# Optimization experiments

Measured on AMD Instinct MI355X. Metric: run time of the kernel, lower is better.

Reference implementation:

```python
import jax, jax.numpy as jnp
import numpy as np

N = 100000   # nodes
E = 1000000  # edges per block
P = 100000   # pos/neg link edges
IN = 128
H = 64


def setup_inputs() -> dict:
    key = jax.random.key(0)
    ks = jax.random.split(key, 24)
    d = {}
    d["x"] = jax.random.normal(ks[0], (N, IN), jnp.float32)
    d["edge_weight"] = jax.random.uniform(ks[1], (3, E), jnp.float32)
    d["src"] = jax.random.randint(ks[2], (E,), 0, N)
    d["dst"] = jax.random.randint(ks[3], (E,), 0, N)
    d["pos_src"] = jax.random.randint(ks[4], (P,), 0, N)
    d["pos_dst"] = jax.random.randint(ks[5], (P,), 0, N)
    d["neg_src"] = jax.random.randint(ks[6], (P,), 0, N)
    d["neg_dst"] = jax.random.randint(ks[7], (P,), 0, N)
    s = 1.0 / np.sqrt(IN)
    h = 1.0 / np.sqrt(H)
    d["W0"] = jax.random.normal(ks[8], (IN, H), jnp.float32) * s
    d["b0"] = jnp.zeros((H,), jnp.float32)
    d["W1"] = jax.random.normal(ks[9], (H, H), jnp.float32) * h
    d["b1"] = jnp.zeros((H,), jnp.float32)
    d["W2"] = jax.random.normal(ks[10], (H, H), jnp.float32) * h
    d["b2"] = jnp.zeros((H,), jnp.float32)
    d["P0"] = jax.random.normal(ks[11], (H, H), jnp.float32) * h
    d["pb0"] = jnp.zeros((H,), jnp.float32)
    d["P1"] = jax.random.normal(ks[12], (H, H), jnp.float32) * h
    d["pb1"] = jnp.zeros((H,), jnp.float32)
    d["P2"] = jax.random.normal(ks[13], (H, 1), jnp.float32) * h
    d["pb2"] = jnp.zeros((1,), jnp.float32)
    return d


def _graph_conv(h, W, b, src, dst, ew, n_nodes):
    # DGL GraphConv, norm='both': D_out^{-1/2} on source feats,
    # edge-weighted sum aggregation, D_in^{-1/2} on result, then linear.
    ones = jnp.ones(src.shape[0], h.dtype)
    deg_out = jax.ops.segment_sum(ones, src, num_segments=n_nodes)
    deg_in = jax.ops.segment_sum(ones, dst, num_segments=n_nodes)
    norm_src = jax.lax.rsqrt(jnp.maximum(deg_out, 1.0))
    norm_dst = jax.lax.rsqrt(jnp.maximum(deg_in, 1.0))
    # apply weight before aggregation (in_feats >= out_feats); math-equivalent either way
    hw = (h * norm_src[:, None]) @ W            # [N, H]
    msg = hw[src] * ew[:, None]                 # [E, H] gather + scale
    agg = jax.ops.segment_sum(msg, dst, num_segments=n_nodes)  # scatter-add
    return agg * norm_dst[:, None] + b


def reference(x, edge_weight, src, dst, pos_src, pos_dst, neg_src, neg_dst,
              W0, b0, W1, b1, W2, b2, P0, pb0, P1, pb1, P2, pb2):
    h = jax.nn.relu(_graph_conv(x, W0, b0, src, dst, edge_weight[0], N))
    h = jax.nn.relu(_graph_conv(h, W1, b1, src, dst, edge_weight[1], N))
    h = _graph_conv(h, W2, b2, src, dst, edge_weight[2], N)  # no relu on last layer

    def mlp(z):
        z = jax.nn.relu(z @ P0 + pb0)
        z = jax.nn.relu(z @ P1 + pb1)
        return z @ P2 + pb2

    h_pos = mlp(h[pos_src] * h[pos_dst])  # [P, 1]
    h_neg = mlp(h[neg_src] * h[neg_dst])  # [P, 1]
    return (h_pos, h_neg)
```

## Files before the change

kernel.cpp:

```cpp
#include <hip/hip_runtime.h>


#define NN 100000
#define NE 1000000
#define NP 100000
#define SCAN_NB 98

__device__ __forceinline__ void row_fma(float4& acc, float xv, const float4& wv) {
    acc.x = fmaf(xv, wv.x, acc.x);
    acc.y = fmaf(xv, wv.y, acc.y);
    acc.z = fmaf(xv, wv.z, acc.z);
    acc.w = fmaf(xv, wv.w, acc.w);
}

__global__ void deg_kernel(const int4* __restrict__ src4, const int4* __restrict__ dst4,
                           int* __restrict__ deg_out, int* __restrict__ deg_in, int E4) {
    int tid = blockIdx.x * blockDim.x + threadIdx.x;
    if (tid < E4) {
        int4 s = src4[tid], d = dst4[tid];
        atomicAdd(&deg_out[s.x], 1);
        atomicAdd(&deg_out[s.y], 1);
        atomicAdd(&deg_out[s.z], 1);
        atomicAdd(&deg_out[s.w], 1);
        atomicAdd(&deg_in[d.x], 1);
        atomicAdd(&deg_in[d.y], 1);
        atomicAdd(&deg_in[d.z], 1);
        atomicAdd(&deg_in[d.w], 1);
    }
}

__global__ void norm_kernel(const int* __restrict__ deg_out, const int* __restrict__ deg_in,
                            float* __restrict__ norm_src, float* __restrict__ norm_dst, int n) {
    int i = blockIdx.x * blockDim.x + threadIdx.x;
    if (i < n) {
        norm_src[i] = rsqrtf(fmaxf((float)deg_out[i], 1.0f));
        norm_dst[i] = rsqrtf(fmaxf((float)deg_in[i], 1.0f));
    }
}

__global__ __launch_bounds__(1024) void scan_block(const int* __restrict__ deg,
                                                   int* __restrict__ tmp_excl,
                                                   int* __restrict__ blocksums, int n) {
    __shared__ int wsums[16];
    const int i = blockIdx.x * 1024 + threadIdx.x;
    const int lane = threadIdx.x & 63, w = threadIdx.x >> 6;
    int v = (i < n) ? deg[i] : 0;
    int s = v;
#pragma unroll
    for (int off = 1; off < 64; off <<= 1) {
        int u = __shfl_up(s, off, 64);
        if (lane >= off) s += u;
    }
    if (lane == 63) wsums[w] = s;
    __syncthreads();
    if (w == 0) {
        int wv = (lane < 16) ? wsums[lane] : 0;
#pragma unroll
        for (int off = 1; off < 16; off <<= 1) {
            int u = __shfl_up(wv, off, 64);
            if (lane >= off) wv += u;
        }
        if (lane < 16) wsums[lane] = wv;
    }
    __syncthreads();
    int excl = s - v + (w > 0 ? wsums[w - 1] : 0);
    if (i < n) tmp_excl[i] = excl;
    if (threadIdx.x == 1023) blocksums[blockIdx.x] = excl + v;
}

__global__ void scan_sums(int* __restrict__ bs, int nb) {
    __shared__ int wtot[2];
    const int t = threadIdx.x;
    const int lane = t & 63, w = t >> 6;
    int v = (t < nb) ? bs[t] : 0;
    int s = v;
#pragma unroll
    for (int off = 1; off < 64; off <<= 1) {
        int u = __shfl_up(s, off, 64);
        if (lane >= off) s += u;
    }
    if (lane == 63) wtot[w] = s;
    __syncthreads();
    int excl = s - v + (w == 1 ? wtot[0] : 0);
    if (t < nb) bs[t] = excl;
}

__global__ __launch_bounds__(1024) void scan_apply(const int* __restrict__ tmp_excl,
                                                   const int* __restrict__ bs,
                                                   int* __restrict__ row_ptr,
                                                   int* __restrict__ cursor, int n) {
    const int i = blockIdx.x * 1024 + threadIdx.x;
    if (i < n) {
        int r = tmp_excl[i] + bs[blockIdx.x];
        row_ptr[i] = r;
        cursor[i] = r;
    }
    if (i == 0) row_ptr[n] = NE;
}

__global__ void csr_fill(const int* __restrict__ src, const int* __restrict__ dst,
                         const float* __restrict__ ew, int* __restrict__ cursor,
                         float4* __restrict__ cedge, int E) {
    int tid = blockIdx.x * blockDim.x + threadIdx.x;
    int stride = gridDim.x * blockDim.x;
    for (int e = tid; e < E; e += stride) {
        int d = dst[e];
        int slot = atomicAdd(&cursor[d], 1);
        float4 c;
        c.x = __int_as_float(src[e]);
        c.y = ew[e];
        c.z = ew[NE + e];
        c.w = ew[2 * NE + e];
        cedge[slot] = c;
    }
}

template <int WSEL, bool FINAL>
__global__ __launch_bounds__(256) void aggregate(const float* __restrict__ hw,
                                                 const float4* __restrict__ cedge,
                                                 const int* __restrict__ row_ptr,
                                                 const float* __restrict__ norm_src,
                                                 const float* __restrict__ norm_dst,
                                                 const float* __restrict__ bias,
                                                 float* __restrict__ outx, int n) {
    const int lane = threadIdx.x & 63;
    const int gw = (blockIdx.x * blockDim.x + threadIdx.x) >> 6;
    const int nw = (gridDim.x * blockDim.x) >> 6;
    const float blane = bias[lane];
    for (int node = gw; node < n; node += nw) {
        int beg = row_ptr[node], end = row_ptr[node + 1];
        float a0 = 0.f, a1 = 0.f, a2 = 0.f, a3 = 0.f;
        int i = beg;
        for (; i + 3 < end; i += 4) {
            float4 c0 = cedge[i], c1 = cedge[i + 1], c2 = cedge[i + 2], c3 = cedge[i + 3];
            int s0 = __float_as_int(c0.x), s1 = __float_as_int(c1.x);
            int s2 = __float_as_int(c2.x), s3 = __float_as_int(c3.x);
            float w0 = (WSEL == 0) ? c0.y : (WSEL == 1) ? c0.z : c0.w;
            float w1 = (WSEL == 0) ? c1.y : (WSEL == 1) ? c1.z : c1.w;
            float w2 = (WSEL == 0) ? c2.y : (WSEL == 1) ? c2.z : c2.w;
            float w3 = (WSEL == 0) ? c3.y : (WSEL == 1) ? c3.z : c3.w;
            a0 = fmaf(hw[s0 * 64 + lane], w0, a0);
            a1 = fmaf(hw[s1 * 64 + lane], w1, a1);
            a2 = fmaf(hw[s2 * 64 + lane], w2, a2);
            a3 = fmaf(hw[s3 * 64 + lane], w3, a3);
        }
        for (; i < end; ++i) {
            float4 c0 = cedge[i];
            int s0 = __float_as_int(c0.x);
            float w0 = (WSEL == 0) ? c0.y : (WSEL == 1) ? c0.z : c0.w;
            a0 = fmaf(hw[s0 * 64 + lane], w0, a0);
        }
        float a = (a0 + a1) + (a2 + a3);
        float nd = norm_dst[node];
        float t;
        if (FINAL) {
            t = fmaf(a, nd, blane);
        } else {
            t = fmaxf(fmaf(a, nd, blane), 0.f) * norm_src[node];
        }
        outx[node * 64 + lane] = t;
    }
}

template <int K, bool SCALE>
__global__ __launch_bounds__(256) void gemm_tile(const float* __restrict__ in,
                                                 const float* __restrict__ W,
                                                 const float* __restrict__ norm_src,
                                                 float* __restrict__ out, int n) {
    __shared__ float Xs[64][K + 4];
    const int tid = threadIdx.x;
    const int ntiles = (n + 63) >> 6;
    const int tr = tid >> 4, tc = tid & 15;

    for (int tile = blockIdx.x; tile < ntiles; tile += gridDim.x) {
        for (int idx = tid; idx < K * 16; idx += 256) {
            int r = idx / (K / 4), kq = idx % (K / 4);
            int row = tile * 64 + r;
            float4 v = make_float4(0.f, 0.f, 0.f, 0.f);
            if (row < n) v = *(const float4*)&in[row * K + kq * 4];
            *(float4*)&Xs[r][kq * 4] = v;
        }
        __syncthreads();

        float4 acc0 = {0, 0, 0, 0}, acc1 = {0, 0, 0, 0}, acc2 = {0, 0, 0, 0}, acc3 = {0, 0, 0, 0};
#pragma unroll 4
        for (int k4 = 0; k4 < K / 4; ++k4) {
            const int kb = k4 * 4;
            float4 xv0 = *(const float4*)&Xs[tr * 4 + 0][kb];
            float4 xv1 = *(const float4*)&Xs[tr * 4 + 1][kb];
            float4 xv2 = *(const float4*)&Xs[tr * 4 + 2][kb];
            float4 xv3 = *(const float4*)&Xs[tr * 4 + 3][kb];
            const float* wb = &W[kb * 64 + tc * 4];
            float4 wk;
            wk = *(const float4*)(wb);
            row_fma(acc0, xv0.x, wk); row_fma(acc1, xv1.x, wk); row_fma(acc2, xv2.x, wk); row_fma(acc3, xv3.x, wk);
            wk = *(const float4*)(wb + 64);
            row_fma(acc0, xv0.y, wk); row_fma(acc1, xv1.y, wk); row_fma(acc2, xv2.y, wk); row_fma(acc3, xv3.y, wk);
            wk = *(const float4*)(wb + 128);
            row_fma(acc0, xv0.z, wk); row_fma(acc1, xv1.z, wk); row_fma(acc2, xv2.z, wk); row_fma(acc3, xv3.z, wk);
            wk = *(const float4*)(wb + 192);
            row_fma(acc0, xv0.w, wk); row_fma(acc1, xv1.w, wk); row_fma(acc2, xv2.w, wk); row_fma(acc3, xv3.w, wk);
        }

#pragma unroll
        for (int i = 0; i < 4; ++i) {
            int row = tile * 64 + tr * 4 + i;
            if (row < n) {
                float4 o = (i == 0) ? acc0 : (i == 1) ? acc1 : (i == 2) ? acc2 : acc3;
                if (SCALE) {
                    float ns = norm_src[row];
                    o.x *= ns; o.y *= ns; o.z *= ns; o.w *= ns;
                }
                *(float4*)&out[row * 64 + tc * 4] = o;
            }
        }
        __syncthreads();
    }
}

#define ZST 76

__global__ __launch_bounds__(256) void mlp_tile(const float* __restrict__ hfin,
                                                const float* __restrict__ P0,
                                                const float* __restrict__ pb0,
                                                const float* __restrict__ P1,
                                                const float* __restrict__ pb1,
                                                const float* __restrict__ P2,
                                                const float* __restrict__ pb2,
                                                const int* __restrict__ pos_src,
                                                const int* __restrict__ pos_dst,
                                                const int* __restrict__ neg_src,
                                                const int* __restrict__ neg_dst,
                                                float* __restrict__ out, int P) {
    __shared__ float Zs[64][ZST];
    __shared__ float pb0s[64], pb1s[64], P2s[64];
    __shared__ int pas[64], pbs[64];
    const int tid = threadIdx.x;
    if (tid < 64) {
        pb0s[tid] = pb0[tid];
        pb1s[tid] = pb1[tid];
        P2s[tid] = P2[tid];
    }
    const float pb2v = pb2[0];
    const int lane = tid & 63, w = tid >> 6;
    const int tr = tid >> 4, tc = tid & 15;
    const int ntiles = (2 * P) >> 6;

    for (int tile = blockIdx.x; tile < ntiles; tile += gridDim.x) {
        const int base = tile << 6;
        __syncthreads();
        if (tid < 64) {
            int p = base + tid;
            pas[tid] = (p < P) ? pos_src[p] : neg_src[p - P];
            pbs[tid] = (p < P) ? pos_dst[p] : neg_dst[p - P];
        }
        __syncthreads();

#pragma unroll 4
        for (int pi = w; pi < 64; pi += 4) {
            float ha = hfin[pas[pi] * 64 + lane];
            float hb = hfin[pbs[pi] * 64 + lane];
            Zs[pi][lane] = ha * hb;
        }
        __syncthreads();

        float4 acc0, acc1, acc2, acc3;
        {
            float4 binit = *(const float4*)&pb0s[tc * 4];
            acc0 = binit; acc1 = binit; acc2 = binit; acc3 = binit;
        }
#pragma unroll 4
        for (int k4 = 0; k4 < 16; ++k4) {
            const int kb = k4 * 4;
            float4 xv0 = *(const float4*)&Zs[tr * 4 + 0][kb];
            float4 xv1 = *(const float4*)&Zs[tr * 4 + 1][kb];
            float4 xv2 = *(const float4*)&Zs[tr * 4 + 2][kb];
            float4 xv3 = *(const float4*)&Zs[tr * 4 + 3][kb];
            const float* wb = &P0[kb * 64 + tc * 4];
            float4 wk;
            wk = *(const float4*)(wb);
            row_fma(acc0, xv0.x, wk); row_fma(acc1, xv1.x, wk); row_fma(acc2, xv2.x, wk); row_fma(acc3, xv3.x, wk);
            wk = *(const float4*)(wb + 64);
            row_fma(acc0, xv0.y, wk); row_fma(acc1, xv1.y, wk); row_fma(acc2, xv2.y, wk); row_fma(acc3, xv3.y, wk);
            wk = *(const float4*)(wb + 128);
            row_fma(acc0, xv0.z, wk); row_fma(acc1, xv1.z, wk); row_fma(acc2, xv2.z, wk); row_fma(acc3, xv3.z, wk);
            wk = *(const float4*)(wb + 192);
            row_fma(acc0, xv0.w, wk); row_fma(acc1, xv1.w, wk); row_fma(acc2, xv2.w, wk); row_fma(acc3, xv3.w, wk);
        }
        __syncthreads();
#pragma unroll
        for (int i = 0; i < 4; ++i) {
            float4 o = (i == 0) ? acc0 : (i == 1) ? acc1 : (i == 2) ? acc2 : acc3;
            o.x = fmaxf(o.x, 0.f); o.y = fmaxf(o.y, 0.f); o.z = fmaxf(o.z, 0.f); o.w = fmaxf(o.w, 0.f);
            *(float4*)&Zs[tr * 4 + i][tc * 4] = o;
        }
        __syncthreads();

        {
            float4 binit = *(const float4*)&pb1s[tc * 4];
            acc0 = binit; acc1 = binit; acc2 = binit; acc3 = binit;
        }
#pragma unroll 4
        for (int k4 = 0; k4 < 16; ++k4) {
            const int kb = k4 * 4;
            float4 xv0 = *(const float4*)&Zs[tr * 4 + 0][kb];
            float4 xv1 = *(const float4*)&Zs[tr * 4 + 1][kb];
            float4 xv2 = *(const float4*)&Zs[tr * 4 + 2][kb];
            float4 xv3 = *(const float4*)&Zs[tr * 4 + 3][kb];
            const float* wb = &P1[kb * 64 + tc * 4];
            float4 wk;
            wk = *(const float4*)(wb);
            row_fma(acc0, xv0.x, wk); row_fma(acc1, xv1.x, wk); row_fma(acc2, xv2.x, wk); row_fma(acc3, xv3.x, wk);
            wk = *(const float4*)(wb + 64);
            row_fma(acc0, xv0.y, wk); row_fma(acc1, xv1.y, wk); row_fma(acc2, xv2.y, wk); row_fma(acc3, xv3.y, wk);
            wk = *(const float4*)(wb + 128);
            row_fma(acc0, xv0.z, wk); row_fma(acc1, xv1.z, wk); row_fma(acc2, xv2.z, wk); row_fma(acc3, xv3.z, wk);
            wk = *(const float4*)(wb + 192);
            row_fma(acc0, xv0.w, wk); row_fma(acc1, xv1.w, wk); row_fma(acc2, xv2.w, wk); row_fma(acc3, xv3.w, wk);
        }
        __syncthreads();
#pragma unroll
        for (int i = 0; i < 4; ++i) {
            float4 o = (i == 0) ? acc0 : (i == 1) ? acc1 : (i == 2) ? acc2 : acc3;
            o.x = fmaxf(o.x, 0.f); o.y = fmaxf(o.y, 0.f); o.z = fmaxf(o.z, 0.f); o.w = fmaxf(o.w, 0.f);
            *(float4*)&Zs[tr * 4 + i][tc * 4] = o;
        }
        __syncthreads();

        {
            int p = tid >> 2, kq = tid & 3;
            float s = 0.f;
#pragma unroll
            for (int i = 0; i < 16; ++i) s = fmaf(Zs[p][kq * 16 + i], P2s[kq * 16 + i], s);
            s += __shfl_xor(s, 1, 64);
            s += __shfl_xor(s, 2, 64);
            if (kq == 0) out[base + p] = s + pb2v;
        }
    }
}

extern "C" void kernel_launch(void* const* d_in, const int* in_sizes, int n_in,
                              void* d_out, int out_size, void* d_ws, size_t ws_size,
                              hipStream_t stream) {
    const float* x     = (const float*)d_in[0];
    const float* ew    = (const float*)d_in[1];
    const int* src     = (const int*)d_in[2];
    const int* dst     = (const int*)d_in[3];
    const int* pos_src = (const int*)d_in[4];
    const int* pos_dst = (const int*)d_in[5];
    const int* neg_src = (const int*)d_in[6];
    const int* neg_dst = (const int*)d_in[7];
    const float* W0    = (const float*)d_in[8];
    const float* b0    = (const float*)d_in[9];
    const float* W1    = (const float*)d_in[10];
    const float* b1    = (const float*)d_in[11];
    const float* W2    = (const float*)d_in[12];
    const float* b2    = (const float*)d_in[13];
    const float* P0    = (const float*)d_in[14];
    const float* pb0   = (const float*)d_in[15];
    const float* P1    = (const float*)d_in[16];
    const float* pb1   = (const float*)d_in[17];
    const float* P2    = (const float*)d_in[18];
    const float* pb2   = (const float*)d_in[19];
    float* out = (float*)d_out;

    float* ws = (float*)d_ws;
    float* norm_src = ws;
    float* norm_dst = ws + 100000;
    int* cursor     = (int*)(ws + 200000);
    int* deg_in     = (int*)(ws + 300000);
    int* row_ptr    = (int*)(ws + 400000);
    float4* cedge   = (float4*)(ws + 500004);
    float* hw       = ws + 4500004;
    float* agg      = ws + 10900004;

    int* tmp_excl  = (int*)hw;
    int* blocksums = (int*)hw + NN;

    hipMemsetAsync(cursor, 0, 2 * NN * sizeof(int), stream);
    deg_kernel<<<(NE / 4 + 255) / 256, 256, 0, stream>>>((const int4*)src, (const int4*)dst,
                                                         cursor, deg_in, NE / 4);
    norm_kernel<<<(NN + 255) / 256, 256, 0, stream>>>(cursor, deg_in, norm_src, norm_dst, NN);
    scan_block<<<SCAN_NB, 1024, 0, stream>>>(deg_in, tmp_excl, blocksums, NN);
    scan_sums<<<1, 128, 0, stream>>>(blocksums, SCAN_NB);
    scan_apply<<<SCAN_NB, 1024, 0, stream>>>(tmp_excl, blocksums, row_ptr, cursor, NN);
    csr_fill<<<2048, 256, 0, stream>>>(src, dst, ew, cursor, cedge, NE);

    const int NT = (NN + 63) / 64;

    gemm_tile<128, true><<<NT, 256, 0, stream>>>(x, W0, norm_src, hw, NN);
    aggregate<0, false><<<4096, 256, 0, stream>>>(hw, cedge, row_ptr, norm_src, norm_dst, b0, agg, NN);
    gemm_tile<64, false><<<NT, 256, 0, stream>>>(agg, W1, nullptr, hw, NN);
    aggregate<1, false><<<4096, 256, 0, stream>>>(hw, cedge, row_ptr, norm_src, norm_dst, b1, agg, NN);
    gemm_tile<64, false><<<NT, 256, 0, stream>>>(agg, W2, nullptr, hw, NN);
    aggregate<2, true><<<4096, 256, 0, stream>>>(hw, cedge, row_ptr, norm_src, norm_dst, b2, agg, NN);

    mlp_tile<<<1024, 256, 0, stream>>>(agg, P0, pb0, P1, pb1, P2, pb2,
                                       pos_src, pos_dst, neg_src, neg_dst, out, NP);
}
```

Measured before the change: 527.2 us.

## Unroll aggregate gathers, stage weights in LDS for GEMM, flatten MLP tiling

The aggregate loop now issues eight independent row gathers per iteration, which raises memory-level parallelism in the edge-gather phase. The node GEMM now stages the weight matrix in shared memory and reads input rows straight from global memory instead of staging an X tile; each block handles exactly one tile and the launch bounds request more occupancy. The MLP kernel launches one block per 64-pair tile instead of using a grid-stride loop, and it batches the gathers of several pairs at once. Reading X directly with float4 loads may give uncoalesced access, since each thread walks its own row.

```diff
diff --git a/kernel.cpp b/kernel.cpp
--- a/kernel.cpp
+++ b/kernel.cpp
@@ -131,24 +131,37 @@
         int beg = row_ptr[node], end = row_ptr[node + 1];
         float a0 = 0.f, a1 = 0.f, a2 = 0.f, a3 = 0.f;
         int i = beg;
-        for (; i + 3 < end; i += 4) {
-            float4 c0 = cedge[i], c1 = cedge[i + 1], c2 = cedge[i + 2], c3 = cedge[i + 3];
-            int s0 = __float_as_int(c0.x), s1 = __float_as_int(c1.x);
-            int s2 = __float_as_int(c2.x), s3 = __float_as_int(c3.x);
-            float w0 = (WSEL == 0) ? c0.y : (WSEL == 1) ? c0.z : c0.w;
-            float w1 = (WSEL == 0) ? c1.y : (WSEL == 1) ? c1.z : c1.w;
-            float w2 = (WSEL == 0) ? c2.y : (WSEL == 1) ? c2.z : c2.w;
-            float w3 = (WSEL == 0) ? c3.y : (WSEL == 1) ? c3.z : c3.w;
-            a0 = fmaf(hw[s0 * 64 + lane], w0, a0);
-            a1 = fmaf(hw[s1 * 64 + lane], w1, a1);
-            a2 = fmaf(hw[s2 * 64 + lane], w2, a2);
-            a3 = fmaf(hw[s3 * 64 + lane], w3, a3);
-        }
-        for (; i < end; ++i) {
+        for (; i + 7 < end; i += 8) {
+            float4 c0 = cedge[i + 0], c1 = cedge[i + 1], c2 = cedge[i + 2], c3 = cedge[i + 3];
+            float4 c4 = cedge[i + 4], c5 = cedge[i + 5], c6 = cedge[i + 6], c7 = cedge[i + 7];
+            float h0 = hw[__float_as_int(c0.x) * 64 + lane];
+            float h1 = hw[__float_as_int(c1.x) * 64 + lane];
+            float h2 = hw[__float_as_int(c2.x) * 64 + lane];
+            float h3 = hw[__float_as_int(c3.x) * 64 + lane];
+            float h4 = hw[__float_as_int(c4.x) * 64 + lane];
+            float h5 = hw[__float_as_int(c5.x) * 64 + lane];
+            float h6 = hw[__float_as_int(c6.x) * 64 + lane];
+            float h7 = hw[__float_as_int(c7.x) * 64 + lane];
+            a0 = fmaf(h0, (WSEL == 0) ? c0.y : (WSEL == 1) ? c0.z : c0.w, a0);
+            a1 = fmaf(h1, (WSEL == 0) ? c1.y : (WSEL == 1) ? c1.z : c1.w, a1);
+            a2 = fmaf(h2, (WSEL == 0) ? c2.y : (WSEL == 1) ? c2.z : c2.w, a2);
+            a3 = fmaf(h3, (WSEL == 0) ? c3.y : (WSEL == 1) ? c3.z : c3.w, a3);
+            a0 = fmaf(h4, (WSEL == 0) ? c4.y : (WSEL == 1) ? c4.z : c4.w, a0);
+            a1 = fmaf(h5, (WSEL == 0) ? c5.y : (WSEL == 1) ? c5.z : c5.w, a1);
+            a2 = fmaf(h6, (WSEL == 0) ? c6.y : (WSEL == 1) ? c6.z : c6.w, a2);
+            a3 = fmaf(h7, (WSEL == 0) ? c7.y : (WSEL == 1) ? c7.z : c7.w, a3);
+        }
+        for (; i + 1 < end; i += 2) {
+            float4 c0 = cedge[i], c1 = cedge[i + 1];
+            float h0 = hw[__float_as_int(c0.x) * 64 + lane];
+            float h1 = hw[__float_as_int(c1.x) * 64 + lane];
+            a0 = fmaf(h0, (WSEL == 0) ? c0.y : (WSEL == 1) ? c0.z : c0.w, a0);
+            a1 = fmaf(h1, (WSEL == 0) ? c1.y : (WSEL == 1) ? c1.z : c1.w, a1);
+        }
+        if (i < end) {
             float4 c0 = cedge[i];
-            int s0 = __float_as_int(c0.x);
-            float w0 = (WSEL == 0) ? c0.y : (WSEL == 1) ? c0.z : c0.w;
-            a0 = fmaf(hw[s0 * 64 + lane], w0, a0);
+            float h0 = hw[__float_as_int(c0.x) * 64 + lane];
+            a0 = fmaf(h0, (WSEL == 0) ? c0.y : (WSEL == 1) ? c0.z : c0.w, a0);
         }
         float a = (a0 + a1) + (a2 + a3);
         float nd = norm_dst[node];
@@ -163,58 +176,53 @@
 }
 
 template <int K, bool SCALE>
-__global__ __launch_bounds__(256) void gemm_tile(const float* __restrict__ in,
-                                                 const float* __restrict__ W,
-                                                 const float* __restrict__ norm_src,
-                                                 float* __restrict__ out, int n) {
-    __shared__ float Xs[64][K + 4];
+__global__ __launch_bounds__(256, 5) void gemm_tile(const float* __restrict__ in,
+                                                    const float* __restrict__ W,
+                                                    const float* __restrict__ norm_src,
+                                                    float* __restrict__ out, int n) {
+    __shared__ float Ws[K * 64];
     const int tid = threadIdx.x;
-    const int ntiles = (n + 63) >> 6;
+    for (int i = tid; i < K * 16; i += 256) ((float4*)Ws)[i] = ((const float4*)W)[i];
+    __syncthreads();
+
     const int tr = tid >> 4, tc = tid & 15;
-
-    for (int tile = blockIdx.x; tile < ntiles; tile += gridDim.x) {
-        for (int idx = tid; idx < K * 16; idx += 256) {
-            int r = idx / (K / 4), kq = idx % (K / 4);
-            int row = tile * 64 + r;
-            float4 v = make_float4(0.f, 0.f, 0.f, 0.f);
-            if (row < n) v = *(const float4*)&in[row * K + kq * 4];
-            *(float4*)&Xs[r][kq * 4] = v;
-        }
-        __syncthreads();
-
-        float4 acc0 = {0, 0, 0, 0}, acc1 = {0, 0, 0, 0}, acc2 = {0, 0, 0, 0}, acc3 = {0, 0, 0, 0};
+    const int row0 = blockIdx.x * 64 + tr * 4;
+    const float* xr0 = in + (size_t)min(row0 + 0, n - 1) * K;
+    const float* xr1 = in + (size_t)min(row0 + 1, n - 1) * K;
+    const float* xr2 = in + (size_t)min(row0 + 2, n - 1) * K;
+    const float* xr3 = in + (size_t)min(row0 + 3, n - 1) * K;
+
+    float4 acc0 = {0, 0, 0, 0}, acc1 = {0, 0, 0, 0}, acc2 = {0, 0, 0, 0}, acc3 = {0, 0, 0, 0};
 #pragma unroll 4
-        for (int k4 = 0; k4 < K / 4; ++k4) {
-            const int kb = k4 * 4;
-            float4 xv0 = *(const float4*)&Xs[tr * 4 + 0][kb];
-            float4 xv1 = *(const float4*)&Xs[tr * 4 + 1][kb];
-            float4 xv2 = *(const float4*)&Xs[tr * 4 + 2][kb];
-            float4 xv3 = *(const float4*)&Xs[tr * 4 + 3][kb];
-            const float* wb = &W[kb * 64 + tc * 4];
-            float4 wk;
-            wk = *(const float4*)(wb);
-            row_fma(acc0, xv0.x, wk); row_fma(acc1, xv1.x, wk); row_fma(acc2, xv2.x, wk); row_fma(acc3, xv3.x, wk);
-            wk = *(const float4*)(wb + 64);
-            row_fma(acc0, xv0.y, wk); row_fma(acc1, xv1.y, wk); row_fma(acc2, xv2.y, wk); row_fma(acc3, xv3.y, wk);
-            wk = *(const float4*)(wb + 128);
-            row_fma(acc0, xv0.z, wk); row_fma(acc1, xv1.z, wk); row_fma(acc2, xv2.z, wk); row_fma(acc3, xv3.z, wk);
-            wk = *(const float4*)(wb + 192);
-            row_fma(acc0, xv0.w, wk); row_fma(acc1, xv1.w, wk); row_fma(acc2, xv2.w, wk); row_fma(acc3, xv3.w, wk);
-        }
-
-#pragma unroll
-        for (int i = 0; i < 4; ++i) {
-            int row = tile * 64 + tr * 4 + i;
-            if (row < n) {
-                float4 o = (i == 0) ? acc0 : (i == 1) ? acc1 : (i == 2) ? acc2 : acc3;
-                if (SCALE) {
-                    float ns = norm_src[row];
-                    o.x *= ns; o.y *= ns; o.z *= ns; o.w *= ns;
-                }
-                *(float4*)&out[row * 64 + tc * 4] = o;
+    for (int k4 = 0; k4 < K / 4; ++k4) {
+        const int kb = k4 * 4;
+        float4 xv0 = *(const float4*)&xr0[kb];
+        float4 xv1 = *(const float4*)&xr1[kb];
+        float4 xv2 = *(const float4*)&xr2[kb];
+        float4 xv3 = *(const float4*)&xr3[kb];
+        const float* wb = &Ws[kb * 64 + tc * 4];
+        float4 wk;
+        wk = *(const float4*)(wb);
+        row_fma(acc0, xv0.x, wk); row_fma(acc1, xv1.x, wk); row_fma(acc2, xv2.x, wk); row_fma(acc3, xv3.x, wk);
+        wk = *(const float4*)(wb + 64);
+        row_fma(acc0, xv0.y, wk); row_fma(acc1, xv1.y, wk); row_fma(acc2, xv2.y, wk); row_fma(acc3, xv3.y, wk);
+        wk = *(const float4*)(wb + 128);
+        row_fma(acc0, xv0.z, wk); row_fma(acc1, xv1.z, wk); row_fma(acc2, xv2.z, wk); row_fma(acc3, xv3.z, wk);
+        wk = *(const float4*)(wb + 192);
+        row_fma(acc0, xv0.w, wk); row_fma(acc1, xv1.w, wk); row_fma(acc2, xv2.w, wk); row_fma(acc3, xv3.w, wk);
+    }
+
+#pragma unroll
+    for (int i = 0; i < 4; ++i) {
+        int row = row0 + i;
+        if (row < n) {
+            float4 o = (i == 0) ? acc0 : (i == 1) ? acc1 : (i == 2) ? acc2 : acc3;
+            if (SCALE) {
+                float ns = norm_src[row];
+                o.x *= ns; o.y *= ns; o.z *= ns; o.w *= ns;
             }
-        }
-        __syncthreads();
+            *(float4*)&out[row * 64 + tc * 4] = o;
+        }
     }
 }
 
@@ -236,106 +244,111 @@
     __shared__ float pb0s[64], pb1s[64], P2s[64];
     __shared__ int pas[64], pbs[64];
     const int tid = threadIdx.x;
+    const int base = blockIdx.x << 6;
     if (tid < 64) {
         pb0s[tid] = pb0[tid];
         pb1s[tid] = pb1[tid];
         P2s[tid] = P2[tid];
+        int p = base + tid;
+        pas[tid] = (p < P) ? pos_src[p] : neg_src[p - P];
+        pbs[tid] = (p < P) ? pos_dst[p] : neg_dst[p - P];
     }
     const float pb2v = pb2[0];
     const int lane = tid & 63, w = tid >> 6;
     const int tr = tid >> 4, tc = tid & 15;
-    const int ntiles = (2 * P) >> 6;
-
-    for (int tile = blockIdx.x; tile < ntiles; tile += gridDim.x) {
-        const int base = tile << 6;
-        __syncthreads();
-        if (tid < 64) {
-            int p = base + tid;
-            pas[tid] = (p < P) ? pos_src[p] : neg_src[p - P];
-            pbs[tid] = (p < P) ? pos_dst[p] : neg_dst[p - P];
-        }
-        __syncthreads();
-
+    __syncthreads();
+
+    {
+        const int p0 = 0 + w, p1 = 4 + w, p2 = 8 + w, p3 = 12 + w;
+#pragma unroll
+        for (int pb = 0; pb < 64; pb += 16) {
+            int a0 = pas[pb + p0], b0 = pbs[pb + p0];
+            int a1 = pas[pb + p1], b1 = pbs[pb + p1];
+            int a2 = pas[pb + p2], b2 = pbs[pb + p2];
+            int a3 = pas[pb + p3], b3 = pbs[pb + p3];
+            float ha0 = hfin[a0 * 64 + lane], hb0 = hfin[b0 * 64 + lane];
+            float ha1 = hfin[a1 * 64 + lane], hb1 = hfin[b1 * 64 + lane];
+            float ha2 = hfin[a2 * 64 + lane], hb2 = hfin[b2 * 64 + lane];
+            float ha3 = hfin[a3 * 64 + lane], hb3 = hfin[b3 * 64 + lane];
+            Zs[pb + p0][lane] = ha0 * hb0;
+            Zs[pb + p1][lane] = ha1 * hb1;
+            Zs[pb + p2][lane] = ha2 * hb2;
+            Zs[pb + p3][lane] = ha3 * hb3;
+        }
+    }
+    __syncthreads();
+
+    float4 acc0, acc1, acc2, acc3;
+    {
+        float4 binit = *(const float4*)&pb0s[tc * 4];
+        acc0 = binit; acc1 = binit; acc2 = binit; acc3 = binit;
+    }
 #pragma unroll 4
-        for (int pi = w; pi < 64; pi += 4) {
-            float ha = hfin[pas[pi] * 64 + lane];
-            float hb = hfin[pbs[pi] * 64 + lane];
-            Zs[pi][lane] = ha * hb;
-        }
-        __syncthreads();
-
-        float4 acc0, acc1, acc2, acc3;
-        {
-            float4 binit = *(const float4*)&pb0s[tc * 4];
-            acc0 = binit; acc1 = binit; acc2 = binit; acc3 = binit;
-        }
+    for (int k4 = 0; k4 < 16; ++k4) {
+        const int kb = k4 * 4;
+        float4 xv0 = *(const float4*)&Zs[tr * 4 + 0][kb];
+        float4 xv1 = *(const float4*)&Zs[tr * 4 + 1][kb];
+        float4 xv2 = *(const float4*)&Zs[tr * 4 + 2][kb];
+        float4 xv3 = *(const float4*)&Zs[tr * 4 + 3][kb];
+        const float* wb = &P0[kb * 64 + tc * 4];
+        float4 wk;
+        wk = *(const float4*)(wb);
+        row_fma(acc0, xv0.x, wk); row_fma(acc1, xv1.x, wk); row_fma(acc2, xv2.x, wk); row_fma(acc3, xv3.x, wk);
+        wk = *(const float4*)(wb + 64);
+        row_fma(acc0, xv0.y, wk); row_fma(acc1, xv1.y, wk); row_fma(acc2, xv2.y, wk); row_fma(acc3, xv3.y, wk);
+        wk = *(const float4*)(wb + 128);
+        row_fma(acc0, xv0.z, wk); row_fma(acc1, xv1.z, wk); row_fma(acc2, xv2.z, wk); row_fma(acc3, xv3.z, wk);
+        wk = *(const float4*)(wb + 192);
+        row_fma(acc0, xv0.w, wk); row_fma(acc1, xv1.w, wk); row_fma(acc2, xv2.w, wk); row_fma(acc3, xv3.w, wk);
+    }
+    __syncthreads();
+#pragma unroll
+    for (int i = 0; i < 4; ++i) {
+        float4 o = (i == 0) ? acc0 : (i == 1) ? acc1 : (i == 2) ? acc2 : acc3;
+        o.x = fmaxf(o.x, 0.f); o.y = fmaxf(o.y, 0.f); o.z = fmaxf(o.z, 0.f); o.w = fmaxf(o.w, 0.f);
+        *(float4*)&Zs[tr * 4 + i][tc * 4] = o;
+    }
+    __syncthreads();
+
+    {
+        float4 binit = *(const float4*)&pb1s[tc * 4];
+        acc0 = binit; acc1 = binit; acc2 = binit; acc3 = binit;
+    }
 #pragma unroll 4
-        for (int k4 = 0; k4 < 16; ++k4) {
-            const int kb = k4 * 4;
-            float4 xv0 = *(const float4*)&Zs[tr * 4 + 0][kb];
-            float4 xv1 = *(const float4*)&Zs[tr * 4 + 1][kb];
-            float4 xv2 = *(const float4*)&Zs[tr * 4 + 2][kb];
-            float4 xv3 = *(const float4*)&Zs[tr * 4 + 3][kb];
-            const float* wb = &P0[kb * 64 + tc * 4];
-            float4 wk;
-            wk = *(const float4*)(wb);
-            row_fma(acc0, xv0.x, wk); row_fma(acc1, xv1.x, wk); row_fma(acc2, xv2.x, wk); row_fma(acc3, xv3.x, wk);
-            wk = *(const float4*)(wb + 64);
-            row_fma(acc0, xv0.y, wk); row_fma(acc1, xv1.y, wk); row_fma(acc2, xv2.y, wk); row_fma(acc3, xv3.y, wk);
-            wk = *(const float4*)(wb + 128);
-            row_fma(acc0, xv0.z, wk); row_fma(acc1, xv1.z, wk); row_fma(acc2, xv2.z, wk); row_fma(acc3, xv3.z, wk);
-            wk = *(const float4*)(wb + 192);
-            row_fma(acc0, xv0.w, wk); row_fma(acc1, xv1.w, wk); row_fma(acc2, xv2.w, wk); row_fma(acc3, xv3.w, wk);
-        }
-        __syncthreads();
-#pragma unroll
-        for (int i = 0; i < 4; ++i) {
-            float4 o = (i == 0) ? acc0 : (i == 1) ? acc1 : (i == 2) ? acc2 : acc3;
-            o.x = fmaxf(o.x, 0.f); o.y = fmaxf(o.y, 0.f); o.z = fmaxf(o.z, 0.f); o.w = fmaxf(o.w, 0.f);
-            *(float4*)&Zs[tr * 4 + i][tc * 4] = o;
-        }
-        __syncthreads();
-
-        {
-            float4 binit = *(const float4*)&pb1s[tc * 4];
-            acc0 = binit; acc1 = binit; acc2 = binit; acc3 = binit;
-        }
-#pragma unroll 4
-        for (int k4 = 0; k4 < 16; ++k4) {
-            const int kb = k4 * 4;
-            float4 xv0 = *(const float4*)&Zs[tr * 4 + 0][kb];
-            float4 xv1 = *(const float4*)&Zs[tr * 4 + 1][kb];
-            float4 xv2 = *(const float4*)&Zs[tr * 4 + 2][kb];
-            float4 xv3 = *(const float4*)&Zs[tr * 4 + 3][kb];
-            const float* wb = &P1[kb * 64 + tc * 4];
-            float4 wk;
-            wk = *(const float4*)(wb);
-            row_fma(acc0, xv0.x, wk); row_fma(acc1, xv1.x, wk); row_fma(acc2, xv2.x, wk); row_fma(acc3, xv3.x, wk);
-            wk = *(const float4*)(wb + 64);
-            row_fma(acc0, xv0.y, wk); row_fma(acc1, xv1.y, wk); row_fma(acc2, xv2.y, wk); row_fma(acc3, xv3.y, wk);
-            wk = *(const float4*)(wb + 128);
-            row_fma(acc0, xv0.z, wk); row_fma(acc1, xv1.z, wk); row_fma(acc2, xv2.z, wk); row_fma(acc3, xv3.z, wk);
-            wk = *(const float4*)(wb + 192);
-            row_fma(acc0, xv0.w, wk); row_fma(acc1, xv1.w, wk); row_fma(acc2, xv2.w, wk); row_fma(acc3, xv3.w, wk);
-        }
-        __syncthreads();
-#pragma unroll
-        for (int i = 0; i < 4; ++i) {
-            float4 o = (i == 0) ? acc0 : (i == 1) ? acc1 : (i == 2) ? acc2 : acc3;
-            o.x = fmaxf(o.x, 0.f); o.y = fmaxf(o.y, 0.f); o.z = fmaxf(o.z, 0.f); o.w = fmaxf(o.w, 0.f);
-            *(float4*)&Zs[tr * 4 + i][tc * 4] = o;
-        }
-        __syncthreads();
-
-        {
-            int p = tid >> 2, kq = tid & 3;
-            float s = 0.f;
-#pragma unroll
-            for (int i = 0; i < 16; ++i) s = fmaf(Zs[p][kq * 16 + i], P2s[kq * 16 + i], s);
-            s += __shfl_xor(s, 1, 64);
-            s += __shfl_xor(s, 2, 64);
-            if (kq == 0) out[base + p] = s + pb2v;
-        }
+    for (int k4 = 0; k4 < 16; ++k4) {
+        const int kb = k4 * 4;
+        float4 xv0 = *(const float4*)&Zs[tr * 4 + 0][kb];
+        float4 xv1 = *(const float4*)&Zs[tr * 4 + 1][kb];
+        float4 xv2 = *(const float4*)&Zs[tr * 4 + 2][kb];
+        float4 xv3 = *(const float4*)&Zs[tr * 4 + 3][kb];
+        const float* wb = &P1[kb * 64 + tc * 4];
+        float4 wk;
+        wk = *(const float4*)(wb);
+        row_fma(acc0, xv0.x, wk); row_fma(acc1, xv1.x, wk); row_fma(acc2, xv2.x, wk); row_fma(acc3, xv3.x, wk);
+        wk = *(const float4*)(wb + 64);
+        row_fma(acc0, xv0.y, wk); row_fma(acc1, xv1.y, wk); row_fma(acc2, xv2.y, wk); row_fma(acc3, xv3.y, wk);
+        wk = *(const float4*)(wb + 128);
+        row_fma(acc0, xv0.z, wk); row_fma(acc1, xv1.z, wk); row_fma(acc2, xv2.z, wk); row_fma(acc3, xv3.z, wk);
+        wk = *(const float4*)(wb + 192);
+        row_fma(acc0, xv0.w, wk); row_fma(acc1, xv1.w, wk); row_fma(acc2, xv2.w, wk); row_fma(acc3, xv3.w, wk);
+    }
+    __syncthreads();
+#pragma unroll
+    for (int i = 0; i < 4; ++i) {
+        float4 o = (i == 0) ? acc0 : (i == 1) ? acc1 : (i == 2) ? acc2 : acc3;
+        o.x = fmaxf(o.x, 0.f); o.y = fmaxf(o.y, 0.f); o.z = fmaxf(o.z, 0.f); o.w = fmaxf(o.w, 0.f);
+        *(float4*)&Zs[tr * 4 + i][tc * 4] = o;
+    }
+    __syncthreads();
+
+    {
+        int p = tid >> 2, kq = tid & 3;
+        float s = 0.f;
+#pragma unroll
+        for (int i = 0; i < 16; ++i) s = fmaf(Zs[p][kq * 16 + i], P2s[kq * 16 + i], s);
+        s += __shfl_xor(s, 1, 64);
+        s += __shfl_xor(s, 2, 64);
+        if (kq == 0) out[base + p] = s + pb2v;
     }
 }
 
@@ -395,6 +408,6 @@
     gemm_tile<64, false><<<NT, 256, 0, stream>>>(agg, W2, nullptr, hw, NN);
     aggregate<2, true><<<4096, 256, 0, stream>>>(hw, cedge, row_ptr, norm_src, norm_dst, b2, agg, NN);
 
-    mlp_tile<<<1024, 256, 0, stream>>>(agg, P0, pb0, P1, pb1, P2, pb2,
-                                       pos_src, pos_dst, neg_src, neg_dst, out, NP);
-}
+    mlp_tile<<<(2 * NP) / 64, 256, 0, stream>>>(agg, P0, pb0, P1, pb1, P2, pb2,
+                                                pos_src, pos_dst, neg_src, neg_dst, out, NP);
+}
```

Result: faster. 484.2 us (-8.1%).
